# Kernel optimization log

Measured on AMD Instinct MI355X. Metric: run time of the kernel, lower is better.

Reference implementation:

```python
import jax, jax.numpy as jnp
import numpy as np

B, C, H, W = 16, 512, 32, 32
NH = 8
HD = C // NH


def setup_inputs() -> dict:
    key = jax.random.key(0)
    k1, k2, k3 = jax.random.split(key, 3)
    x = jax.random.normal(k1, (B, C, H, W), dtype=jnp.float32)
    w_qkv = jax.random.normal(k2, (3 * C, C), dtype=jnp.float32) * (1.0 / np.sqrt(C))
    w_proj = jax.random.normal(k3, (C, C), dtype=jnp.float32) * (1.0 / np.sqrt(C))
    b_proj = jnp.zeros((C,), dtype=jnp.float32)
    return {"x": x, "w_qkv": w_qkv, "w_proj": w_proj, "b_proj": b_proj}


def reference(x, w_qkv, w_proj, b_proj):
    b, c, h, w = x.shape
    n = h * w
    # 1x1 conv qkv: (3C, C) applied per pixel
    qkv = jnp.einsum('oc,bchw->bohw', w_qkv, x)  # [B, 3C, H, W]
    qkv = qkv.reshape(b, 3, NH, HD, n)           # [B, 3, nh, hd, N]
    qkv = jnp.transpose(qkv, (1, 0, 2, 4, 3))    # [3, B, nh, N, hd]
    q, k, v = qkv[0], qkv[1], qkv[2]
    scale = HD ** -0.5
    scores = jnp.einsum('bhnd,bhmd->bhnm', q, k) * scale  # [B, nh, N, N]
    attn = jax.nn.softmax(scores, axis=-1)
    out = jnp.einsum('bhnm,bhmd->bhnd', attn, v)          # [B, nh, N, hd]
    out = jnp.transpose(out, (0, 1, 3, 2)).reshape(b, c, h, w)
    # 1x1 conv proj with bias
    out = jnp.einsum('oc,bchw->bohw', w_proj, out) + b_proj[None, :, None, None]
    return out
```

## Files before the change

### kernel.cpp

```cpp
#include <hip/hip_runtime.h>
#include <hip/hip_bf16.h>
#include <math.h>

#define BB 16
#define CC 512
#define NH 8
#define HD 64
#define NN 1024
#define THREEC 1536

#define QSCALE 0.18033688f

typedef __attribute__((ext_vector_type(8))) short bf16x8;
typedef __attribute__((ext_vector_type(4))) float f32x4;
typedef __attribute__((ext_vector_type(16))) float f32x16;

#if __has_builtin(__builtin_amdgcn_exp2f)
#define EXP2F __builtin_amdgcn_exp2f
#else
#define EXP2F exp2f
#endif

#define XT_OFF 0u
#define WQ_OFF 16777216u
#define WP_OFF 18350080u
#define QB_OFF 18874368u
#define KB_OFF 35651584u
#define VT_OFF 52428800u
#define AB_OFF 69206016u

static __device__ inline unsigned short f2bf(float f) {
  union { float f; unsigned u; } v; v.f = f;
  unsigned r = v.u + 0x7fffu + ((v.u >> 16) & 1u);
  return (unsigned short)(r >> 16);
}

static __device__ inline unsigned pk2bf(float a, float b) {
#if defined(__AMDGCN__) && __has_builtin(__builtin_amdgcn_cvt_pk_bf16_f32)
  typedef __attribute__((ext_vector_type(2))) __bf16 bfp2;
  union { bfp2 v; unsigned u; } z;
  z.v = __builtin_amdgcn_cvt_pk_bf16_f32(a, b);
  return z.u;
#else
  return (unsigned)f2bf(a) | ((unsigned)f2bf(b) << 16);
#endif
}

static __device__ inline void gld_lds16(const unsigned short* g, unsigned short* l) {
  __builtin_amdgcn_global_load_lds(
      (const __attribute__((address_space(1))) unsigned int*)g,
      (__attribute__((address_space(3))) unsigned int*)l, 16, 0, 0);
}

__global__ __launch_bounds__(256) void prep_w(const float* __restrict__ wqkv,
                                              const float* __restrict__ wproj,
                                              unsigned short* __restrict__ dq,
                                              unsigned short* __restrict__ dp) {
  const size_t i8 = ((size_t)blockIdx.x * 256 + threadIdx.x) * 8;
  const float* src;
  unsigned short* dst;
  if (i8 < 786432u) { src = wqkv + i8; dst = dq + i8; }
  else              { src = wproj + (i8 - 786432u); dst = dp + (i8 - 786432u); }
  float4 a = *(const float4*)src;
  float4 b = *(const float4*)(src + 4);
  unsigned short pk[8] = {f2bf(a.x), f2bf(a.y), f2bf(a.z), f2bf(a.w),
                          f2bf(b.x), f2bf(b.y), f2bf(b.z), f2bf(b.w)};
  *(uint4*)dst = *(const uint4*)pk;
}

__global__ __launch_bounds__(256) void prep_xT(const float* __restrict__ x,
                                               unsigned short* __restrict__ xT) {
  const int b  = blockIdx.z;
  const int c0 = blockIdx.y * 64;
  const int n0 = blockIdx.x * 64;
  __shared__ float tile[64][65];
  const int t  = threadIdx.x;
  const int cl = t >> 4, n4 = (t & 15) * 4;
#pragma unroll
  for (int r = 0; r < 4; ++r) {
    float4 v = *(const float4*)&x[((size_t)b * CC + c0 + cl + 16 * r) * NN + n0 + n4];
    *(float4*)&tile[cl + 16 * r][n4] = v;
  }
  __syncthreads();
  const int nl = t >> 4, c4 = (t & 15) * 4;
#pragma unroll
  for (int r = 0; r < 4; ++r) {
    ushort4 p;
    p.x = f2bf(tile[c4 + 0][nl + 16 * r]);
    p.y = f2bf(tile[c4 + 1][nl + 16 * r]);
    p.z = f2bf(tile[c4 + 2][nl + 16 * r]);
    p.w = f2bf(tile[c4 + 3][nl + 16 * r]);
    *(ushort4*)&xT[((size_t)b * NN + n0 + nl + 16 * r) * CC + c0 + c4] = p;
  }
}

__global__ __launch_bounds__(256) void qkv_mfma(const unsigned short* __restrict__ wq,
                                                const unsigned short* __restrict__ xT,
                                                unsigned short* __restrict__ qb,
                                                unsigned short* __restrict__ kb_,
                                                unsigned short* __restrict__ vt) {
  const int b  = blockIdx.z;
  const int o0 = blockIdx.y * 128;
  const int n0 = blockIdx.x * 128;
  const int t  = threadIdx.x;
  const int w    = t >> 6;
  const int lane = t & 63;
  const int quad = lane >> 4;
  const int l16  = lane & 15;
  const int m_off = (w >> 1) * 64;
  const int n_off = (w & 1) * 64;

  __shared__ unsigned short sm[17408];
  unsigned short* As = sm;
  unsigned short* Bs = sm + 8192;

  const int which = o0 >> 9;
  const bool vmode = (which == 2);

  const int srow = lane >> 3;
  const int ssw  = ((lane & 7) ^ srow) * 8;
  const unsigned short* gA = wq + (size_t)(o0 + 32 * w + srow) * CC + ssw;
  const unsigned short* gB = xT + ((size_t)b * NN + n0 + 32 * w + srow) * CC + ssw;

  f32x4 acc[4][4] = {};

  for (int c0 = 0; c0 < CC; c0 += 64) {
    __syncthreads();
#pragma unroll
    for (int L = 0; L < 4; ++L) {
      gld_lds16(gA + (size_t)(8 * L) * CC + c0, &As[(32 * w + 8 * L) * 64]);
      gld_lds16(gB + (size_t)(8 * L) * CC + c0, &Bs[(32 * w + 8 * L) * 64]);
    }
    __syncthreads();
    const unsigned short* Af = vmode ? Bs : As;
    const unsigned short* Bf = vmode ? As : Bs;
#pragma unroll
    for (int ks = 0; ks < 2; ++ks) {
      const int ph = ((ks * 4 + quad) ^ (l16 & 7)) * 8;
      bf16x8 af[4], bfr[4];
#pragma unroll
      for (int i = 0; i < 4; ++i) {
        af[i]  = *(const bf16x8*)&Af[(m_off + 16 * i + l16) * 64 + ph];
        bfr[i] = *(const bf16x8*)&Bf[(n_off + 16 * i + l16) * 64 + ph];
      }
#pragma unroll
      for (int i = 0; i < 4; ++i)
#pragma unroll
        for (int j = 0; j < 4; ++j)
          acc[i][j] = __builtin_amdgcn_mfma_f32_16x16x32_bf16(af[i], bfr[j], acc[i][j], 0, 0, 0);
    }
  }

  __syncthreads();
  const float sc = (which == 0) ? QSCALE : 1.0f;
#pragma unroll
  for (int i = 0; i < 4; ++i) {
#pragma unroll
    for (int j = 0; j < 4; ++j) {
      const int Drow = m_off + 16 * i + quad * 4;
      const int Dcol = n_off + 16 * j + l16;
      ushort4 p;
      p.x = f2bf(acc[i][j][0] * sc);
      p.y = f2bf(acc[i][j][1] * sc);
      p.z = f2bf(acc[i][j][2] * sc);
      p.w = f2bf(acc[i][j][3] * sc);
      *(ushort4*)&sm[Dcol * 136 + Drow] = p;
    }
  }
  __syncthreads();
  const int lrow = t >> 1;
  const int half = t & 1;
  const unsigned short* src = &sm[lrow * 136 + 64 * half];
  if (!vmode) {
    const int hh = ((o0 >> 6) & 7) + half;
    unsigned short* dst = (which == 0 ? qb : kb_) +
        ((size_t)(b * NH + hh) * NN + n0 + lrow) * HD;
#pragma unroll
    for (int i = 0; i < 8; ++i) *(uint4*)(dst + 8 * i) = *(const uint4*)(src + 8 * i);
  } else {
    const int hh = ((o0 + lrow) >> 6) & 7;
    const int d  = lrow & 63;
    unsigned short* dst = vt + ((size_t)(b * NH + hh) * HD + d) * NN + n0 + 64 * half;
#pragma unroll
    for (int i = 0; i < 8; ++i) *(uint4*)(dst + 8 * i) = *(const uint4*)(src + 8 * i);
  }
}

__global__ __launch_bounds__(256) void attn_mfma(const unsigned short* __restrict__ Qg,
                                                 const unsigned short* __restrict__ Kg,
                                                 const unsigned short* __restrict__ Vtg,
                                                 unsigned short* __restrict__ attnB) {
  const int bh = blockIdx.x;
  const int b  = bh >> 3;
  const int h  = bh & 7;
  const int n0 = blockIdx.y * 128;
  const int t  = threadIdx.x;
  const int w    = t >> 6;
  const int lane = t & 63;
  const int l31  = lane & 31;
  const int hi   = lane >> 5;

  __shared__ unsigned short sm[16384];

  const unsigned short* qrow = Qg + ((size_t)bh * NN + n0 + w * 32 + l31) * HD + hi * 8;
  bf16x8 qf[4];
#pragma unroll
  for (int c = 0; c < 4; ++c) qf[c] = *(const bf16x8*)(qrow + 16 * c);

  const int krow = (l31 & ~12) | ((l31 & 4) << 1) | ((l31 & 8) >> 1);
  const int ksw  = krow & 7;
  const int vsw  = l31 & 7;

  const f32x16 fz = {};
  const short ONE = 0x3F80;
  const bf16x8 onesv = {ONE, ONE, ONE, ONE, ONE, ONE, ONE, ONE};

  f32x16 oacc[2] = {};
  f32x16 lacc = {};

  const int srow = lane >> 3;
  const int sgrp = (lane & 7) ^ (srow & 7);
  const unsigned short* kstage = Kg + (size_t)bh * NN * HD +
                                 (size_t)(16 * w + srow) * HD + sgrp * 8;
  const unsigned short* vstage = Vtg + (size_t)bh * HD * NN +
                                 (size_t)(16 * w + srow) * NN + sgrp * 8;
  const int kso0 = (16 * w) * 64;
  const int kso1 = (16 * w + 8) * 64;

  auto stage = [&](int j0, int p) {
    unsigned short* Kp = sm + p * 8192;
    unsigned short* Vp = Kp + 4096;
    gld_lds16(kstage + (size_t)j0 * HD, Kp + kso0);
    gld_lds16(kstage + (size_t)(j0 + 8) * HD, Kp + kso1);
    gld_lds16(vstage + j0, Vp + kso0);
    gld_lds16(vstage + (size_t)8 * NN + j0, Vp + kso1);
  };

  stage(0, 0);
  int cur = 0;

#pragma unroll 1
  for (int j0 = 0; j0 < NN; j0 += 64) {
    __syncthreads();
    if (j0 + 64 < NN) stage(j0 + 64, cur ^ 1);

    const unsigned short* Ks = sm + cur * 8192;
    const unsigned short* Vt = Ks + 4096;

#pragma unroll
    for (int kb = 0; kb < 2; ++kb) {
      const unsigned short* krp = &Ks[(32 * kb + krow) * 64];
      __builtin_amdgcn_s_setprio(1);
      bf16x8 kf0 = *(const bf16x8*)(krp + (((0 + hi) ^ ksw) * 8));
      f32x16 st = __builtin_amdgcn_mfma_f32_32x32x16_bf16(kf0, qf[0], fz, 0, 0, 0);
#pragma unroll
      for (int c = 1; c < 4; ++c) {
        bf16x8 kf = *(const bf16x8*)(krp + (((2 * c + hi) ^ ksw) * 8));
        st = __builtin_amdgcn_mfma_f32_32x32x16_bf16(kf, qf[c], st, 0, 0, 0);
      }
      __builtin_amdgcn_s_setprio(0);
      unsigned P[8];
#pragma unroll
      for (int i = 0; i < 8; ++i)
        P[i] = pk2bf(EXP2F(st[2 * i]), EXP2F(st[2 * i + 1]));

      __builtin_amdgcn_s_setprio(1);
#pragma unroll
      for (int g = 0; g < 2; ++g) {
        union { unsigned u[4]; bf16x8 v; } cv;
        cv.u[0] = P[4 * g + 0]; cv.u[1] = P[4 * g + 1];
        cv.u[2] = P[4 * g + 2]; cv.u[3] = P[4 * g + 3];
        lacc = __builtin_amdgcn_mfma_f32_32x32x16_bf16(onesv, cv.v, lacc, 0, 0, 0);
#pragma unroll
        for (int mt = 0; mt < 2; ++mt) {
          const int vrow = 32 * mt + l31;
          bf16x8 vf = *(const bf16x8*)&Vt[vrow * 64 + (((4 * kb + 2 * g + hi) ^ vsw) * 8)];
          oacc[mt] = __builtin_amdgcn_mfma_f32_32x32x16_bf16(vf, cv.v, oacc[mt], 0, 0, 0);
        }
      }
      __builtin_amdgcn_s_setprio(0);
    }
    cur ^= 1;
  }

  const float inv = 1.0f / lacc[0];

  __syncthreads();
  unsigned short* Es = sm + w * 2304;
#pragma unroll
  for (int mt = 0; mt < 2; ++mt) {
#pragma unroll
    for (int rr = 0; rr < 4; ++rr) {
      const int d = 32 * mt + 8 * rr + 4 * hi;
      ushort4 p;
      p.x = f2bf(oacc[mt][4 * rr + 0] * inv);
      p.y = f2bf(oacc[mt][4 * rr + 1] * inv);
      p.z = f2bf(oacc[mt][4 * rr + 2] * inv);
      p.w = f2bf(oacc[mt][4 * rr + 3] * inv);
      *(ushort4*)&Es[l31 * 72 + d] = p;
    }
  }
  const int q    = lane >> 1;
  const int half = lane & 1;
  const unsigned short* src = &Es[q * 72 + 32 * half];
  unsigned short* gdst = attnB + ((size_t)b * NN + n0 + w * 32 + q) * CC + h * HD + 32 * half;
#pragma unroll
  for (int i = 0; i < 4; ++i) *(uint4*)(gdst + 8 * i) = *(const uint4*)(src + 8 * i);
}

__global__ __launch_bounds__(256) void proj_mfma(const unsigned short* __restrict__ wp,
                                                 const unsigned short* __restrict__ aB,
                                                 const float* __restrict__ bias,
                                                 float* __restrict__ out) {
  const int b  = blockIdx.z;
  const int o0 = blockIdx.y * 128;
  const int n0 = blockIdx.x * 128;
  const int t  = threadIdx.x;
  const int w    = t >> 6;
  const int lane = t & 63;
  const int quad = lane >> 4;
  const int l16  = lane & 15;
  const int m_off = (w >> 1) * 64;
  const int n_off = (w & 1) * 64;

  __shared__ unsigned short sm[16384];
  unsigned short* As = sm;
  unsigned short* Bs = sm + 8192;

  const int srow = lane >> 3;
  const int ssw  = ((lane & 7) ^ srow) * 8;
  const unsigned short* gA = wp + (size_t)(o0 + 32 * w + srow) * CC + ssw;
  const unsigned short* gB = aB + ((size_t)b * NN + n0 + 32 * w + srow) * CC + ssw;

  f32x4 acc[4][4] = {};

  for (int c0 = 0; c0 < CC; c0 += 64) {
    __syncthreads();
#pragma unroll
    for (int L = 0; L < 4; ++L) {
      gld_lds16(gA + (size_t)(8 * L) * CC + c0, &As[(32 * w + 8 * L) * 64]);
      gld_lds16(gB + (size_t)(8 * L) * CC + c0, &Bs[(32 * w + 8 * L) * 64]);
    }
    __syncthreads();
#pragma unroll
    for (int ks = 0; ks < 2; ++ks) {
      const int ph = ((ks * 4 + quad) ^ (l16 & 7)) * 8;
      bf16x8 af[4], bfr[4];
#pragma unroll
      for (int i = 0; i < 4; ++i) {
        af[i]  = *(const bf16x8*)&As[(m_off + 16 * i + l16) * 64 + ph];
        bfr[i] = *(const bf16x8*)&Bs[(n_off + 16 * i + l16) * 64 + ph];
      }
#pragma unroll
      for (int i = 0; i < 4; ++i)
#pragma unroll
        for (int j = 0; j < 4; ++j)
          acc[i][j] = __builtin_amdgcn_mfma_f32_16x16x32_bf16(af[i], bfr[j], acc[i][j], 0, 0, 0);
    }
  }

#pragma unroll
  for (int i = 0; i < 4; ++i) {
#pragma unroll
    for (int r = 0; r < 4; ++r) {
      const int o = o0 + m_off + 16 * i + quad * 4 + r;
      const float bv = bias[o];
      float* orow = out + ((size_t)b * CC + o) * NN + n0 + n_off;
#pragma unroll
      for (int j = 0; j < 4; ++j)
        orow[16 * j + l16] = acc[i][j][r] + bv;
    }
  }
}

extern "C" void kernel_launch(void* const* d_in, const int* in_sizes, int n_in,
                              void* d_out, int out_size, void* d_ws, size_t ws_size,
                              hipStream_t stream) {
  const float* x      = (const float*)d_in[0];
  const float* w_qkv  = (const float*)d_in[1];
  const float* w_proj = (const float*)d_in[2];
  const float* b_proj = (const float*)d_in[3];
  char* wsb  = (char*)d_ws;
  float* out = (float*)d_out;

  unsigned short* xT  = (unsigned short*)(wsb + XT_OFF);
  unsigned short* wq  = (unsigned short*)(wsb + WQ_OFF);
  unsigned short* wp  = (unsigned short*)(wsb + WP_OFF);
  unsigned short* qb  = (unsigned short*)(wsb + QB_OFF);
  unsigned short* kb_ = (unsigned short*)(wsb + KB_OFF);
  unsigned short* vt  = (unsigned short*)(wsb + VT_OFF);
  unsigned short* aB  = (unsigned short*)(wsb + AB_OFF);

  prep_w<<<512, 256, 0, stream>>>(w_qkv, w_proj, wq, wp);
  prep_xT<<<dim3(16, 8, BB), 256, 0, stream>>>(x, xT);
  qkv_mfma<<<dim3(8, 12, BB), 256, 0, stream>>>(wq, xT, qb, kb_, vt);
  attn_mfma<<<dim3(BB * NH, NN / 128), 256, 0, stream>>>(qb, kb_, vt, aB);
  proj_mfma<<<dim3(8, 4, BB), 256, 0, stream>>>(wp, aB, b_proj, out);
}
```

Before: 194.6 us.

## Software-pipeline QK and PV across key blocks, compute row sums with VALU

Restructures the attention inner loop so that the QK^T MFMAs of the current key block are interleaved with the PV MFMAs of the previous block, staging K one block ahead and V with a one-block lag in separate LDS buffers. The softmax exponentials of one block can then overlap with matrix work on the other. It also drops the ones-vector MFMA used for row sums and instead accumulates the exp values in scalar registers, reducing across the two half-waves with a shuffle. This raises register pressure, since two P tiles are held live, and adds prologue and epilogue stages.

```diff
diff --git a/kernel.cpp b/kernel.cpp
--- a/kernel.cpp
+++ b/kernel.cpp
@@ -212,11 +212,9 @@
   const int vsw  = l31 & 7;
 
   const f32x16 fz = {};
-  const short ONE = 0x3F80;
-  const bf16x8 onesv = {ONE, ONE, ONE, ONE, ONE, ONE, ONE, ONE};
 
   f32x16 oacc[2] = {};
-  f32x16 lacc = {};
+  float lx = 0.f, ly = 0.f;
 
   const int srow = lane >> 3;
   const int sgrp = (lane & 7) ^ (srow & 7);
@@ -227,65 +225,99 @@
   const int kso0 = (16 * w) * 64;
   const int kso1 = (16 * w + 8) * 64;
 
-  auto stage = [&](int j0, int p) {
-    unsigned short* Kp = sm + p * 8192;
-    unsigned short* Vp = Kp + 4096;
+  auto stageK = [&](int j0, int p) {
+    unsigned short* Kp = sm + p * 4096;
     gld_lds16(kstage + (size_t)j0 * HD, Kp + kso0);
     gld_lds16(kstage + (size_t)(j0 + 8) * HD, Kp + kso1);
+  };
+  auto stageV = [&](int j0, int p) {
+    unsigned short* Vp = sm + 8192 + p * 4096;
     gld_lds16(vstage + j0, Vp + kso0);
     gld_lds16(vstage + (size_t)8 * NN + j0, Vp + kso1);
   };
 
-  stage(0, 0);
-  int cur = 0;
+  auto QK = [&](const unsigned short* Ks, int kb) -> f32x16 {
+    const unsigned short* krp = &Ks[(32 * kb + krow) * 64];
+    bf16x8 kf0 = *(const bf16x8*)(krp + (((0 + hi) ^ ksw) * 8));
+    f32x16 st = __builtin_amdgcn_mfma_f32_32x32x16_bf16(kf0, qf[0], fz, 0, 0, 0);
+#pragma unroll
+    for (int c = 1; c < 4; ++c) {
+      bf16x8 kf = *(const bf16x8*)(krp + (((2 * c + hi) ^ ksw) * 8));
+      st = __builtin_amdgcn_mfma_f32_32x32x16_bf16(kf, qf[c], st, 0, 0, 0);
+    }
+    return st;
+  };
+  auto SM = [&](const f32x16& st, unsigned* P) {
+#pragma unroll
+    for (int i = 0; i < 8; ++i) {
+      float ea = EXP2F(st[2 * i]);
+      float eb = EXP2F(st[2 * i + 1]);
+      lx += ea; ly += eb;
+      P[i] = pk2bf(ea, eb);
+    }
+  };
+  auto PV = [&](const unsigned* P, const unsigned short* Vp, int kb) {
+#pragma unroll
+    for (int g = 0; g < 2; ++g) {
+      union { unsigned u[4]; bf16x8 v; } cv;
+      cv.u[0] = P[4 * g + 0]; cv.u[1] = P[4 * g + 1];
+      cv.u[2] = P[4 * g + 2]; cv.u[3] = P[4 * g + 3];
+#pragma unroll
+      for (int mt = 0; mt < 2; ++mt) {
+        const int vrow = 32 * mt + l31;
+        bf16x8 vf = *(const bf16x8*)&Vp[vrow * 64 + (((4 * kb + 2 * g + hi) ^ vsw) * 8)];
+        oacc[mt] = __builtin_amdgcn_mfma_f32_32x32x16_bf16(vf, cv.v, oacc[mt], 0, 0, 0);
+      }
+    }
+  };
+
+  unsigned P0[8], P1[8];
+
+  stageK(0, 0);
+  __syncthreads();
+  stageK(64, 1);
+  stageV(0, 0);
+  {
+    f32x16 st = QK(sm, 0);
+    SM(st, P0);
+    st = QK(sm, 1);
+    SM(st, P1);
+  }
 
 #pragma unroll 1
-  for (int j0 = 0; j0 < NN; j0 += 64) {
+  for (int i = 1; i < 16; ++i) {
     __syncthreads();
-    if (j0 + 64 < NN) stage(j0 + 64, cur ^ 1);
-
-    const unsigned short* Ks = sm + cur * 8192;
-    const unsigned short* Vt = Ks + 4096;
-
-#pragma unroll
-    for (int kb = 0; kb < 2; ++kb) {
-      const unsigned short* krp = &Ks[(32 * kb + krow) * 64];
-      __builtin_amdgcn_s_setprio(1);
-      bf16x8 kf0 = *(const bf16x8*)(krp + (((0 + hi) ^ ksw) * 8));
-      f32x16 st = __builtin_amdgcn_mfma_f32_32x32x16_bf16(kf0, qf[0], fz, 0, 0, 0);
-#pragma unroll
-      for (int c = 1; c < 4; ++c) {
-        bf16x8 kf = *(const bf16x8*)(krp + (((2 * c + hi) ^ ksw) * 8));
-        st = __builtin_amdgcn_mfma_f32_32x32x16_bf16(kf, qf[c], st, 0, 0, 0);
-      }
-      __builtin_amdgcn_s_setprio(0);
-      unsigned P[8];
-#pragma unroll
-      for (int i = 0; i < 8; ++i)
-        P[i] = pk2bf(EXP2F(st[2 * i]), EXP2F(st[2 * i + 1]));
-
-      __builtin_amdgcn_s_setprio(1);
-#pragma unroll
-      for (int g = 0; g < 2; ++g) {
-        union { unsigned u[4]; bf16x8 v; } cv;
-        cv.u[0] = P[4 * g + 0]; cv.u[1] = P[4 * g + 1];
-        cv.u[2] = P[4 * g + 2]; cv.u[3] = P[4 * g + 3];
-        lacc = __builtin_amdgcn_mfma_f32_32x32x16_bf16(onesv, cv.v, lacc, 0, 0, 0);
-#pragma unroll
-        for (int mt = 0; mt < 2; ++mt) {
-          const int vrow = 32 * mt + l31;
-          bf16x8 vf = *(const bf16x8*)&Vt[vrow * 64 + (((4 * kb + 2 * g + hi) ^ vsw) * 8)];
-          oacc[mt] = __builtin_amdgcn_mfma_f32_32x32x16_bf16(vf, cv.v, oacc[mt], 0, 0, 0);
-        }
-      }
-      __builtin_amdgcn_s_setprio(0);
-    }
-    cur ^= 1;
-  }
-
-  const float inv = 1.0f / lacc[0];
+    if (i < 15) stageK(64 * (i + 1), (i + 1) & 1);
+    stageV(64 * i, i & 1);
+    const unsigned short* Ks = sm + (i & 1) * 4096;
+    const unsigned short* Vp = sm + 8192 + ((i - 1) & 1) * 4096;
+
+    __builtin_amdgcn_s_setprio(1);
+    f32x16 st = QK(Ks, 0);
+    PV(P0, Vp, 0);
+    __builtin_amdgcn_s_setprio(0);
+    SM(st, P0);
+
+    __builtin_amdgcn_s_setprio(1);
+    st = QK(Ks, 1);
+    PV(P1, Vp, 1);
+    __builtin_amdgcn_s_setprio(0);
+    SM(st, P1);
+  }
 
   __syncthreads();
+  {
+    const unsigned short* Vp = sm + 8192 + 4096;
+    __builtin_amdgcn_s_setprio(1);
+    PV(P0, Vp, 0);
+    PV(P1, Vp, 1);
+    __builtin_amdgcn_s_setprio(0);
+  }
+
+  float lsum = lx + ly;
+  lsum += __shfl_xor(lsum, 32);
+  const float inv = 1.0f / lsum;
+
   unsigned short* Es = sm + w * 2304;
 #pragma unroll
   for (int mt = 0; mt < 2; ++mt) {
```

After: 191.2 us. No clear change (-1.8%).

## Process two query tiles per wave in attention and sum softmax denominators in VALU

Applied to the files above, without the earlier changes.

Each attention block now covers 256 queries instead of 128, with each wave holding two 32-row query fragments. Every K/V fragment read from LDS therefore feeds two MFMA chains, which halves K/V staging and LDS reads per query. The row-sum MFMA against a ones vector is replaced by scalar accumulation of the exponentials plus a cross-half shuffle, removing one MFMA per group. In exchange the grid is halved to 512 blocks, register pressure roughly doubles (launch bounds now ask for 2 blocks per SM), and the denominator now sums fp32 values rather than the bf16-rounded ones used in the numerator.

```diff
diff --git a/kernel.cpp b/kernel.cpp
--- a/kernel.cpp
+++ b/kernel.cpp
@@ -186,14 +186,14 @@
   }
 }
 
-__global__ __launch_bounds__(256) void attn_mfma(const unsigned short* __restrict__ Qg,
-                                                 const unsigned short* __restrict__ Kg,
-                                                 const unsigned short* __restrict__ Vtg,
-                                                 unsigned short* __restrict__ attnB) {
+__global__ __launch_bounds__(256, 2) void attn_mfma(const unsigned short* __restrict__ Qg,
+                                                    const unsigned short* __restrict__ Kg,
+                                                    const unsigned short* __restrict__ Vtg,
+                                                    unsigned short* __restrict__ attnB) {
   const int bh = blockIdx.x;
   const int b  = bh >> 3;
   const int h  = bh & 7;
-  const int n0 = blockIdx.y * 128;
+  const int n0 = blockIdx.y * 256;
   const int t  = threadIdx.x;
   const int w    = t >> 6;
   const int lane = t & 63;
@@ -202,21 +202,21 @@
 
   __shared__ unsigned short sm[16384];
 
-  const unsigned short* qrow = Qg + ((size_t)bh * NN + n0 + w * 32 + l31) * HD + hi * 8;
-  bf16x8 qf[4];
-#pragma unroll
-  for (int c = 0; c < 4; ++c) qf[c] = *(const bf16x8*)(qrow + 16 * c);
+  const unsigned short* qrow = Qg + ((size_t)bh * NN + n0 + w * 64 + l31) * HD + hi * 8;
+  bf16x8 qfA[4], qfB[4];
+#pragma unroll
+  for (int c = 0; c < 4; ++c) {
+    qfA[c] = *(const bf16x8*)(qrow + 16 * c);
+    qfB[c] = *(const bf16x8*)(qrow + 32 * HD + 16 * c);
+  }
 
   const int krow = (l31 & ~12) | ((l31 & 4) << 1) | ((l31 & 8) >> 1);
   const int ksw  = krow & 7;
   const int vsw  = l31 & 7;
 
   const f32x16 fz = {};
-  const short ONE = 0x3F80;
-  const bf16x8 onesv = {ONE, ONE, ONE, ONE, ONE, ONE, ONE, ONE};
-
-  f32x16 oacc[2] = {};
-  f32x16 lacc = {};
+  f32x16 oaccA[2] = {}, oaccB[2] = {};
+  float lxA = 0.f, lyA = 0.f, lxB = 0.f, lyB = 0.f;
 
   const int srow = lane >> 3;
   const int sgrp = (lane & 7) ^ (srow & 7);
@@ -228,8 +228,8 @@
   const int kso1 = (16 * w + 8) * 64;
 
   auto stage = [&](int j0, int p) {
-    unsigned short* Kp = sm + p * 8192;
-    unsigned short* Vp = Kp + 4096;
+    unsigned short* Kp = sm + p * 4096;
+    unsigned short* Vp = sm + 8192 + p * 4096;
     gld_lds16(kstage + (size_t)j0 * HD, Kp + kso0);
     gld_lds16(kstage + (size_t)(j0 + 8) * HD, Kp + kso1);
     gld_lds16(vstage + j0, Vp + kso0);
@@ -244,38 +244,53 @@
     __syncthreads();
     if (j0 + 64 < NN) stage(j0 + 64, cur ^ 1);
 
-    const unsigned short* Ks = sm + cur * 8192;
-    const unsigned short* Vt = Ks + 4096;
+    const unsigned short* Ks = sm + cur * 4096;
+    const unsigned short* Vt = sm + 8192 + cur * 4096;
 
 #pragma unroll
     for (int kb = 0; kb < 2; ++kb) {
       const unsigned short* krp = &Ks[(32 * kb + krow) * 64];
       __builtin_amdgcn_s_setprio(1);
       bf16x8 kf0 = *(const bf16x8*)(krp + (((0 + hi) ^ ksw) * 8));
-      f32x16 st = __builtin_amdgcn_mfma_f32_32x32x16_bf16(kf0, qf[0], fz, 0, 0, 0);
+      f32x16 stA = __builtin_amdgcn_mfma_f32_32x32x16_bf16(kf0, qfA[0], fz, 0, 0, 0);
+      f32x16 stB = __builtin_amdgcn_mfma_f32_32x32x16_bf16(kf0, qfB[0], fz, 0, 0, 0);
 #pragma unroll
       for (int c = 1; c < 4; ++c) {
         bf16x8 kf = *(const bf16x8*)(krp + (((2 * c + hi) ^ ksw) * 8));
-        st = __builtin_amdgcn_mfma_f32_32x32x16_bf16(kf, qf[c], st, 0, 0, 0);
+        stA = __builtin_amdgcn_mfma_f32_32x32x16_bf16(kf, qfA[c], stA, 0, 0, 0);
+        stB = __builtin_amdgcn_mfma_f32_32x32x16_bf16(kf, qfB[c], stB, 0, 0, 0);
       }
       __builtin_amdgcn_s_setprio(0);
-      unsigned P[8];
-#pragma unroll
-      for (int i = 0; i < 8; ++i)
-        P[i] = pk2bf(EXP2F(st[2 * i]), EXP2F(st[2 * i + 1]));
+      unsigned PA[8], PB[8];
+#pragma unroll
+      for (int i = 0; i < 8; ++i) {
+        float ea = EXP2F(stA[2 * i]);
+        float eb = EXP2F(stA[2 * i + 1]);
+        lxA += ea; lyA += eb;
+        PA[i] = pk2bf(ea, eb);
+      }
+#pragma unroll
+      for (int i = 0; i < 8; ++i) {
+        float ea = EXP2F(stB[2 * i]);
+        float eb = EXP2F(stB[2 * i + 1]);
+        lxB += ea; lyB += eb;
+        PB[i] = pk2bf(ea, eb);
+      }
 
       __builtin_amdgcn_s_setprio(1);
 #pragma unroll
       for (int g = 0; g < 2; ++g) {
-        union { unsigned u[4]; bf16x8 v; } cv;
-        cv.u[0] = P[4 * g + 0]; cv.u[1] = P[4 * g + 1];
-        cv.u[2] = P[4 * g + 2]; cv.u[3] = P[4 * g + 3];
-        lacc = __builtin_amdgcn_mfma_f32_32x32x16_bf16(onesv, cv.v, lacc, 0, 0, 0);
+        union { unsigned u[4]; bf16x8 v; } cvA, cvB;
+        cvA.u[0] = PA[4 * g + 0]; cvA.u[1] = PA[4 * g + 1];
+        cvA.u[2] = PA[4 * g + 2]; cvA.u[3] = PA[4 * g + 3];
+        cvB.u[0] = PB[4 * g + 0]; cvB.u[1] = PB[4 * g + 1];
+        cvB.u[2] = PB[4 * g + 2]; cvB.u[3] = PB[4 * g + 3];
 #pragma unroll
         for (int mt = 0; mt < 2; ++mt) {
           const int vrow = 32 * mt + l31;
           bf16x8 vf = *(const bf16x8*)&Vt[vrow * 64 + (((4 * kb + 2 * g + hi) ^ vsw) * 8)];
-          oacc[mt] = __builtin_amdgcn_mfma_f32_32x32x16_bf16(vf, cv.v, oacc[mt], 0, 0, 0);
+          oaccA[mt] = __builtin_amdgcn_mfma_f32_32x32x16_bf16(vf, cvA.v, oaccA[mt], 0, 0, 0);
+          oaccB[mt] = __builtin_amdgcn_mfma_f32_32x32x16_bf16(vf, cvB.v, oaccB[mt], 0, 0, 0);
         }
       }
       __builtin_amdgcn_s_setprio(0);
@@ -283,29 +298,56 @@
     cur ^= 1;
   }
 
-  const float inv = 1.0f / lacc[0];
+  float lsA = lxA + lyA;
+  lsA += __shfl_xor(lsA, 32);
+  const float invA = 1.0f / lsA;
+  float lsB = lxB + lyB;
+  lsB += __shfl_xor(lsB, 32);
+  const float invB = 1.0f / lsB;
 
   __syncthreads();
   unsigned short* Es = sm + w * 2304;
+  const int q    = lane >> 1;
+  const int half = lane & 1;
+  const unsigned short* esrc = &Es[q * 72 + 32 * half];
+
 #pragma unroll
   for (int mt = 0; mt < 2; ++mt) {
 #pragma unroll
     for (int rr = 0; rr < 4; ++rr) {
       const int d = 32 * mt + 8 * rr + 4 * hi;
       ushort4 p;
-      p.x = f2bf(oacc[mt][4 * rr + 0] * inv);
-      p.y = f2bf(oacc[mt][4 * rr + 1] * inv);
-      p.z = f2bf(oacc[mt][4 * rr + 2] * inv);
-      p.w = f2bf(oacc[mt][4 * rr + 3] * inv);
+      p.x = f2bf(oaccA[mt][4 * rr + 0] * invA);
+      p.y = f2bf(oaccA[mt][4 * rr + 1] * invA);
+      p.z = f2bf(oaccA[mt][4 * rr + 2] * invA);
+      p.w = f2bf(oaccA[mt][4 * rr + 3] * invA);
       *(ushort4*)&Es[l31 * 72 + d] = p;
     }
   }
-  const int q    = lane >> 1;
-  const int half = lane & 1;
-  const unsigned short* src = &Es[q * 72 + 32 * half];
-  unsigned short* gdst = attnB + ((size_t)b * NN + n0 + w * 32 + q) * CC + h * HD + 32 * half;
-#pragma unroll
-  for (int i = 0; i < 4; ++i) *(uint4*)(gdst + 8 * i) = *(const uint4*)(src + 8 * i);
+  {
+    unsigned short* gdst = attnB + ((size_t)b * NN + n0 + w * 64 + q) * CC + h * HD + 32 * half;
+#pragma unroll
+    for (int i = 0; i < 4; ++i) *(uint4*)(gdst + 8 * i) = *(const uint4*)(esrc + 8 * i);
+  }
+
+#pragma unroll
+  for (int mt = 0; mt < 2; ++mt) {
+#pragma unroll
+    for (int rr = 0; rr < 4; ++rr) {
+      const int d = 32 * mt + 8 * rr + 4 * hi;
+      ushort4 p;
+      p.x = f2bf(oaccB[mt][4 * rr + 0] * invB);
+      p.y = f2bf(oaccB[mt][4 * rr + 1] * invB);
+      p.z = f2bf(oaccB[mt][4 * rr + 2] * invB);
+      p.w = f2bf(oaccB[mt][4 * rr + 3] * invB);
+      *(ushort4*)&Es[l31 * 72 + d] = p;
+    }
+  }
+  {
+    unsigned short* gdst = attnB + ((size_t)b * NN + n0 + w * 64 + 32 + q) * CC + h * HD + 32 * half;
+#pragma unroll
+    for (int i = 0; i < 4; ++i) *(uint4*)(gdst + 8 * i) = *(const uint4*)(esrc + 8 * i);
+  }
 }
 
 __global__ __launch_bounds__(256) void proj_mfma(const unsigned short* __restrict__ wp,
@@ -394,6 +436,6 @@
   prep_w<<<512, 256, 0, stream>>>(w_qkv, w_proj, wq, wp);
   prep_xT<<<dim3(16, 8, BB), 256, 0, stream>>>(x, xT);
   qkv_mfma<<<dim3(8, 12, BB), 256, 0, stream>>>(wq, xT, qb, kb_, vt);
-  attn_mfma<<<dim3(BB * NH, NN / 128), 256, 0, stream>>>(qb, kb_, vt, aB);
+  attn_mfma<<<dim3(BB * NH, NN / 256), 256, 0, stream>>>(qb, kb_, vt, aB);
   proj_mfma<<<dim3(8, 4, BB), 256, 0, stream>>>(wp, aB, b_proj, out);
 }
```

Result: no change. 191.5 us (-1.6%).
